# Kernel tuning notes

Hardware: AMD Instinct MI355X
Metric: run time of the kernel (lower is better)

Reference implementation:

```python
import jax, jax.numpy as jnp
import numpy as np
from jax import lax


def setup_inputs() -> dict:
    key = jax.random.key(0)
    k1, k2 = jax.random.split(key)
    C, H, W = 64, 224, 224
    C_out, hf, wf = 128, 3, 3
    x = jax.random.normal(k1, (C, H, W), dtype=jnp.float32)
    kernels = jax.random.normal(k2, (C_out, C, hf, wf), dtype=jnp.float32)
    return {"x": x, "kernels": kernels}


def reference(x, kernels):
    # Original builds im2col columns per output pixel then does k_col @ x_col,
    # i.e. a cross-correlation with 'valid' padding and stride 1.
    # lax.conv_general_dilated computes exactly this (no kernel flip).
    stride = 1
    out = lax.conv_general_dilated(
        x[None],                       # (1, C, H, W) NCHW
        kernels,                       # (C_out, C_in, hf, wf) OIHW
        window_strides=(stride, stride),
        padding="VALID",
        dimension_numbers=("NCHW", "OIHW", "NCHW"),
    )
    return out[0]                      # (C_out, H_out, W_out)
```

## Files before the change

kernel.cpp:

```cpp
#include <hip/hip_runtime.h>
#include <hip/hip_bf16.h>


#define H_IN   224
#define W_IN   224
#define C_OUT  128
#define H_OUT  222
#define W_OUT  222
#define XP     226
#define CPAD   72
#define TW     68

typedef __attribute__((ext_vector_type(8)))  short bf16x8;
typedef __attribute__((ext_vector_type(16))) float f32x16;

static __device__ __forceinline__ unsigned short f2bs(float f) {
    union { __hip_bfloat16 h; unsigned short u; } cv;
    cv.h = __float2bfloat16(f);
    return cv.u;
}

__global__ __launch_bounds__(256)
void transform_w_kernel(const float* __restrict__ w, __hip_bfloat16* __restrict__ wt)
{
    int idx = blockIdx.x * 256 + threadIdx.x;
    if (idx < 9 * 128 * 64) {
        int ij  = idx >> 13;
        int rem = idx & 8191;
        int co  = rem >> 6;
        int c   = rem & 63;
        wt[((ij * 8 + (c >> 3)) * 128 + co) * 8 + (c & 7)] =
            __float2bfloat16(w[(co * 64 + c) * 9 + ij]);
    }
}

__global__ __launch_bounds__(256)
void transpose_x_kernel(const float* __restrict__ x, __hip_bfloat16* __restrict__ xt)
{
    __shared__ __align__(16) unsigned short tile[64 * TW];
    const int h  = blockIdx.y;
    const int w0 = blockIdx.x * 64;
    const int t  = threadIdx.x;

    {
        const int wq = (t & 15) * 4;
        const int c0 = t >> 4;
        #pragma unroll
        for (int p = 0; p < 4; ++p) {
            const int c  = c0 + p * 16;
            const int wg = w0 + wq;
            float4 v = make_float4(0.f, 0.f, 0.f, 0.f);
            if (h < H_IN && wg < W_IN)
                v = *(const float4*)(x + ((size_t)c * H_IN + h) * W_IN + wg);
            ushort4 b;
            b.x = f2bs(v.x); b.y = f2bs(v.y); b.z = f2bs(v.z); b.w = f2bs(v.w);
            *(ushort4*)(tile + c * TW + wq) = b;
        }
    }
    __syncthreads();

    {
        const int wl = t >> 2;
        const int cq = (t & 3) * 16;
        const int wg = w0 + wl;
        if (wg < XP) {
            alignas(16) unsigned short r[16];
            #pragma unroll
            for (int k = 0; k < 16; ++k)
                r[k] = tile[(cq + k) * TW + wl];
            float4* d = (float4*)((unsigned short*)xt + ((size_t)h * XP + wg) * 64 + cq);
            d[0] = ((const float4*)r)[0];
            d[1] = ((const float4*)r)[1];
        }
    }
}

__global__ __launch_bounds__(256)
void conv_mfma_kernel(const __hip_bfloat16* __restrict__ xt,
                      const __hip_bfloat16* __restrict__ wt,
                      float* __restrict__ out)
{
    __shared__ __hip_bfloat16 xs[10 * 34 * CPAD];
    __shared__ __hip_bfloat16 wsb[2][8 * 64 * 8];
    const int ow0 = blockIdx.x * 32;
    const int oh0 = blockIdx.y * 8;
    const int co0 = blockIdx.z * 64;
    const int tid = threadIdx.x;

    for (int q = tid; q < 10 * 34 * 8; q += 256) {
        int sub = q & 7;
        int pix = q >> 3;
        int row = pix / 34;
        int wc  = pix - row * 34;
        *(float4*)(xs + (row * 34 + wc) * CPAD + sub * 8) =
            *(const float4*)(xt + ((oh0 + row) * XP + (ow0 + wc)) * 64 + sub * 8);
    }
    {
        const float4* s = (const float4*)(wt + (size_t)co0 * 8);
        #pragma unroll
        for (int k = 0; k < 2; ++k) {
            int q  = k * 256 + tid;
            int ks = q >> 6;
            int cc = q & 63;
            *(float4*)(&wsb[0][(ks * 64 + cc) * 8]) =
                *(const float4*)(wt + ((0 * 8 + ks) * 128 + co0 + cc) * 8);
        }
        (void)s;
    }
    __syncthreads();

    const int wave = tid >> 6;
    const int lane = tid & 63;
    const int n    = lane & 31;
    const int h    = lane >> 5;
    const int r0   = wave * 2;

    f32x16 acc[2][2] = {};

    #pragma unroll
    for (int p = 0; p < 9; ++p) {
        const int i  = p / 3;
        const int jj = p - i * 3;
        const int cb = p & 1;

        float4 pf[2];
        int ks0 = 0, cc0 = 0, ks1 = 0, cc1 = 0;
        if (p < 8) {
            #pragma unroll
            for (int k = 0; k < 2; ++k) {
                int q  = k * 256 + tid;
                int ks = q >> 6;
                int cc = q & 63;
                pf[k] = *(const float4*)(wt + (((p + 1) * 8 + ks) * 128 + co0 + cc) * 8);
                if (k == 0) { ks0 = ks; cc0 = cc; } else { ks1 = ks; cc1 = cc; }
            }
        }

        #pragma unroll
        for (int t = 0; t < 4; ++t) {
            bf16x8 afr[2], bfr[2];
            #pragma unroll
            for (int mi = 0; mi < 2; ++mi)
                afr[mi] = *(const bf16x8*)(&wsb[cb][((t * 2 + h) * 64 + mi * 32 + n) * 8]);
            #pragma unroll
            for (int ni = 0; ni < 2; ++ni)
                bfr[ni] = *(const bf16x8*)(xs +
                    ((i + r0 + ni) * 34 + n + jj) * CPAD + t * 16 + h * 8);
            #pragma unroll
            for (int mi = 0; mi < 2; ++mi)
                #pragma unroll
                for (int ni = 0; ni < 2; ++ni)
                    acc[mi][ni] = __builtin_amdgcn_mfma_f32_32x32x16_bf16(
                        afr[mi], bfr[ni], acc[mi][ni], 0, 0, 0);
        }

        if (p < 8) {
            *(float4*)(&wsb[1 - cb][(ks0 * 64 + cc0) * 8]) = pf[0];
            *(float4*)(&wsb[1 - cb][(ks1 * 64 + cc1) * 8]) = pf[1];
        }
        __syncthreads();
    }

    #pragma unroll
    for (int mi = 0; mi < 2; ++mi) {
        #pragma unroll
        for (int ni = 0; ni < 2; ++ni) {
            const int oh = oh0 + r0 + ni;
            const int ow = ow0 + n;
            if (oh < H_OUT && ow < W_OUT) {
                #pragma unroll
                for (int r = 0; r < 16; ++r) {
                    int co = co0 + mi * 32 + (r & 3) + 8 * (r >> 2) + 4 * h;
                    out[(size_t)co * (H_OUT * W_OUT) + oh * W_OUT + ow] = acc[mi][ni][r];
                }
            }
        }
    }
}

extern "C" void kernel_launch(void* const* d_in, const int* in_sizes, int n_in,
                              void* d_out, int out_size, void* d_ws, size_t ws_size,
                              hipStream_t stream)
{
    const float* x = (const float*)d_in[0];
    const float* w = (const float*)d_in[1];
    float* out     = (float*)d_out;

    __hip_bfloat16* xt = (__hip_bfloat16*)d_ws;
    __hip_bfloat16* wt = (__hip_bfloat16*)((char*)d_ws + (size_t)XP * XP * 64 * 2);

    transform_w_kernel<<<288, 256, 0, stream>>>(w, wt);
    transpose_x_kernel<<<dim3(4, XP), 256, 0, stream>>>(x, xt);
    conv_mfma_kernel<<<dim3(7, 28, 2), 256, 0, stream>>>(xt, wt, out);
}
```

Measured before the change: 88.64 us.

## Fuse weight/input preprocessing and conv into one cooperative kernel with grid sync

Merges the weight transform, input transpose and MFMA convolution kernels into a single cooperative launch of 512 blocks. The blocks first grid-stride over the preprocessing work units, reusing the shared-memory tile buffer, then a grid-wide sync separates that phase from the conv phase, which runs on the first 392 blocks. This removes two kernel launches and the gaps between them. In exchange it adds a grid barrier, requires co-residency (launch bounds of 2 blocks per CU), and leaves blocks idle during the conv phase.

Result: slower. 166.0 us (+87.3%).

```diff
diff --git a/kernel.cpp b/kernel.cpp
--- a/kernel.cpp
+++ b/kernel.cpp
@@ -1,5 +1,8 @@
 #include <hip/hip_runtime.h>
 #include <hip/hip_bf16.h>
+#include <hip/hip_cooperative_groups.h>
+
+namespace cg = cooperative_groups;
 
 
 #define H_IN   224
@@ -11,6 +14,11 @@
 #define CPAD   72
 #define TW     68
 
+#define PREP_W_UNITS 288
+#define PREP_UNITS   1192
+#define CONV_UNITS   392
+#define GRID_BLKS    512
+
 typedef __attribute__((ext_vector_type(8)))  short bf16x8;
 typedef __attribute__((ext_vector_type(16))) float f32x16;
 
@@ -20,72 +28,76 @@
     return cv.u;
 }
 
-__global__ __launch_bounds__(256)
-void transform_w_kernel(const float* __restrict__ w, __hip_bfloat16* __restrict__ wt)
+__global__ __launch_bounds__(256, 2)
+void fused_conv_kernel(const float* __restrict__ x, const float* __restrict__ w,
+                       __hip_bfloat16* __restrict__ xt, __hip_bfloat16* __restrict__ wt,
+                       float* __restrict__ out)
 {
-    int idx = blockIdx.x * 256 + threadIdx.x;
-    if (idx < 9 * 128 * 64) {
-        int ij  = idx >> 13;
-        int rem = idx & 8191;
-        int co  = rem >> 6;
-        int c   = rem & 63;
-        wt[((ij * 8 + (c >> 3)) * 128 + co) * 8 + (c & 7)] =
-            __float2bfloat16(w[(co * 64 + c) * 9 + ij]);
-    }
-}
-
-__global__ __launch_bounds__(256)
-void transpose_x_kernel(const float* __restrict__ x, __hip_bfloat16* __restrict__ xt)
-{
-    __shared__ __align__(16) unsigned short tile[64 * TW];
-    const int h  = blockIdx.y;
-    const int w0 = blockIdx.x * 64;
-    const int t  = threadIdx.x;
-
-    {
-        const int wq = (t & 15) * 4;
-        const int c0 = t >> 4;
-        #pragma unroll
-        for (int p = 0; p < 4; ++p) {
-            const int c  = c0 + p * 16;
-            const int wg = w0 + wq;
-            float4 v = make_float4(0.f, 0.f, 0.f, 0.f);
-            if (h < H_IN && wg < W_IN)
-                v = *(const float4*)(x + ((size_t)c * H_IN + h) * W_IN + wg);
-            ushort4 b;
-            b.x = f2bs(v.x); b.y = f2bs(v.y); b.z = f2bs(v.z); b.w = f2bs(v.w);
-            *(ushort4*)(tile + c * TW + wq) = b;
-        }
-    }
-    __syncthreads();
-
-    {
-        const int wl = t >> 2;
-        const int cq = (t & 3) * 16;
-        const int wg = w0 + wl;
-        if (wg < XP) {
-            alignas(16) unsigned short r[16];
-            #pragma unroll
-            for (int k = 0; k < 16; ++k)
-                r[k] = tile[(cq + k) * TW + wl];
-            float4* d = (float4*)((unsigned short*)xt + ((size_t)h * XP + wg) * 64 + cq);
-            d[0] = ((const float4*)r)[0];
-            d[1] = ((const float4*)r)[1];
-        }
-    }
-}
-
-__global__ __launch_bounds__(256)
-void conv_mfma_kernel(const __hip_bfloat16* __restrict__ xt,
-                      const __hip_bfloat16* __restrict__ wt,
-                      float* __restrict__ out)
-{
-    __shared__ __hip_bfloat16 xs[10 * 34 * CPAD];
-    __shared__ __hip_bfloat16 wsb[2][8 * 64 * 8];
-    const int ow0 = blockIdx.x * 32;
-    const int oh0 = blockIdx.y * 8;
-    const int co0 = blockIdx.z * 64;
+    __shared__ __align__(16) __hip_bfloat16 xs[10 * 34 * CPAD];
+    __shared__ __align__(16) __hip_bfloat16 wsb[2][8 * 64 * 8];
     const int tid = threadIdx.x;
+
+    for (int u = blockIdx.x; u < PREP_UNITS; u += GRID_BLKS) {
+        if (u < PREP_W_UNITS) {
+            int idx = u * 256 + tid;
+            int ij  = idx >> 13;
+            int rem = idx & 8191;
+            int co  = rem >> 6;
+            int c   = rem & 63;
+            wt[((ij * 8 + (c >> 3)) * 128 + co) * 8 + (c & 7)] =
+                __float2bfloat16(w[(co * 64 + c) * 9 + ij]);
+        } else {
+            unsigned short* tile = (unsigned short*)xs;
+            const int ux = u - PREP_W_UNITS;
+            const int h  = ux >> 2;
+            const int w0 = (ux & 3) * 64;
+            __syncthreads();
+
+            {
+                const int wq = (tid & 15) * 4;
+                const int c0 = tid >> 4;
+                #pragma unroll
+                for (int p = 0; p < 4; ++p) {
+                    const int c  = c0 + p * 16;
+                    const int wg = w0 + wq;
+                    float4 v = make_float4(0.f, 0.f, 0.f, 0.f);
+                    if (h < H_IN && wg < W_IN)
+                        v = *(const float4*)(x + ((size_t)c * H_IN + h) * W_IN + wg);
+                    ushort4 b;
+                    b.x = f2bs(v.x); b.y = f2bs(v.y); b.z = f2bs(v.z); b.w = f2bs(v.w);
+                    *(ushort4*)(tile + c * TW + wq) = b;
+                }
+            }
+            __syncthreads();
+
+            {
+                const int wl = tid >> 2;
+                const int cq = (tid & 3) * 16;
+                const int wg = w0 + wl;
+                if (wg < XP) {
+                    alignas(16) unsigned short r[16];
+                    #pragma unroll
+                    for (int k = 0; k < 16; ++k)
+                        r[k] = tile[(cq + k) * TW + wl];
+                    float4* d = (float4*)((unsigned short*)xt + ((size_t)h * XP + wg) * 64 + cq);
+                    d[0] = ((const float4*)r)[0];
+                    d[1] = ((const float4*)r)[1];
+                }
+            }
+        }
+    }
+
+    cg::this_grid().sync();
+
+    const int u = blockIdx.x;
+    if (u >= CONV_UNITS) return;
+    const int bz  = u / 196;
+    const int rm  = u - bz * 196;
+    const int by  = rm / 7;
+    const int bx  = rm - by * 7;
+    const int ow0 = bx * 32;
+    const int oh0 = by * 8;
+    const int co0 = bz * 64;
 
     for (int q = tid; q < 10 * 34 * 8; q += 256) {
         int sub = q & 7;
@@ -95,17 +107,13 @@
         *(float4*)(xs + (row * 34 + wc) * CPAD + sub * 8) =
             *(const float4*)(xt + ((oh0 + row) * XP + (ow0 + wc)) * 64 + sub * 8);
     }
-    {
-        const float4* s = (const float4*)(wt + (size_t)co0 * 8);
-        #pragma unroll
-        for (int k = 0; k < 2; ++k) {
-            int q  = k * 256 + tid;
-            int ks = q >> 6;
-            int cc = q & 63;
-            *(float4*)(&wsb[0][(ks * 64 + cc) * 8]) =
-                *(const float4*)(wt + ((0 * 8 + ks) * 128 + co0 + cc) * 8);
-        }
-        (void)s;
+    #pragma unroll
+    for (int k = 0; k < 2; ++k) {
+        int q  = k * 256 + tid;
+        int ks = q >> 6;
+        int cc = q & 63;
+        *(float4*)(&wsb[0][(ks * 64 + cc) * 8]) =
+            *(const float4*)(wt + ((0 * 8 + ks) * 128 + co0 + cc) * 8);
     }
     __syncthreads();
 
@@ -189,7 +197,7 @@
     __hip_bfloat16* xt = (__hip_bfloat16*)d_ws;
     __hip_bfloat16* wt = (__hip_bfloat16*)((char*)d_ws + (size_t)XP * XP * 64 * 2);
 
-    transform_w_kernel<<<288, 256, 0, stream>>>(w, wt);
-    transpose_x_kernel<<<dim3(4, XP), 256, 0, stream>>>(x, xt);
-    conv_mfma_kernel<<<dim3(7, 28, 2), 256, 0, stream>>>(xt, wt, out);
+    void* args[] = { (void*)&x, (void*)&w, (void*)&xt, (void*)&wt, (void*)&out };
+    hipLaunchCooperativeKernel(fused_conv_kernel, dim3(GRID_BLKS), dim3(256),
+                               args, 0, stream);
 }
```

## Halve output-row tile, load weights directly from global, drop LDS weight buffer

Applied to the files above, without the earlier changes.

The conv kernel now handles 4 output rows per block instead of 8, doubling the grid, and each wave computes one row instead of two. Weight fragments are read straight from global memory (cached) instead of being double-buffered through shared memory, which removes the per-tap __syncthreads barriers. A launch bounds occupancy hint is added. The aim is higher occupancy and less synchronisation, at the cost of more halo reloads, fewer MFMAs per weight load and global-latency weight fetches in the inner loop.

Measured after the change: 88.01 us. About the same (-0.7%).

```diff
diff --git a/kernel.cpp b/kernel.cpp
--- a/kernel.cpp
+++ b/kernel.cpp
@@ -75,19 +75,18 @@
     }
 }
 
-__global__ __launch_bounds__(256)
+__global__ __launch_bounds__(256, 4)
 void conv_mfma_kernel(const __hip_bfloat16* __restrict__ xt,
                       const __hip_bfloat16* __restrict__ wt,
                       float* __restrict__ out)
 {
-    __shared__ __hip_bfloat16 xs[10 * 34 * CPAD];
-    __shared__ __hip_bfloat16 wsb[2][8 * 64 * 8];
+    __shared__ __hip_bfloat16 xs[6 * 34 * CPAD];
     const int ow0 = blockIdx.x * 32;
-    const int oh0 = blockIdx.y * 8;
+    const int oh0 = blockIdx.y * 4;
     const int co0 = blockIdx.z * 64;
     const int tid = threadIdx.x;
 
-    for (int q = tid; q < 10 * 34 * 8; q += 256) {
+    for (int q = tid; q < 6 * 34 * 8; q += 256) {
         int sub = q & 7;
         int pix = q >> 3;
         int row = pix / 34;
@@ -95,84 +94,44 @@
         *(float4*)(xs + (row * 34 + wc) * CPAD + sub * 8) =
             *(const float4*)(xt + ((oh0 + row) * XP + (ow0 + wc)) * 64 + sub * 8);
     }
-    {
-        const float4* s = (const float4*)(wt + (size_t)co0 * 8);
-        #pragma unroll
-        for (int k = 0; k < 2; ++k) {
-            int q  = k * 256 + tid;
-            int ks = q >> 6;
-            int cc = q & 63;
-            *(float4*)(&wsb[0][(ks * 64 + cc) * 8]) =
-                *(const float4*)(wt + ((0 * 8 + ks) * 128 + co0 + cc) * 8);
-        }
-        (void)s;
-    }
     __syncthreads();
 
     const int wave = tid >> 6;
     const int lane = tid & 63;
     const int n    = lane & 31;
     const int h    = lane >> 5;
-    const int r0   = wave * 2;
 
-    f32x16 acc[2][2] = {};
+    f32x16 acc[2] = {};
 
     #pragma unroll
     for (int p = 0; p < 9; ++p) {
         const int i  = p / 3;
         const int jj = p - i * 3;
-        const int cb = p & 1;
-
-        float4 pf[2];
-        int ks0 = 0, cc0 = 0, ks1 = 0, cc1 = 0;
-        if (p < 8) {
-            #pragma unroll
-            for (int k = 0; k < 2; ++k) {
-                int q  = k * 256 + tid;
-                int ks = q >> 6;
-                int cc = q & 63;
-                pf[k] = *(const float4*)(wt + (((p + 1) * 8 + ks) * 128 + co0 + cc) * 8);
-                if (k == 0) { ks0 = ks; cc0 = cc; } else { ks1 = ks; cc1 = cc; }
-            }
-        }
-
         #pragma unroll
         for (int t = 0; t < 4; ++t) {
-            bf16x8 afr[2], bfr[2];
+            bf16x8 afr[2];
             #pragma unroll
             for (int mi = 0; mi < 2; ++mi)
-                afr[mi] = *(const bf16x8*)(&wsb[cb][((t * 2 + h) * 64 + mi * 32 + n) * 8]);
-            #pragma unroll
-            for (int ni = 0; ni < 2; ++ni)
-                bfr[ni] = *(const bf16x8*)(xs +
-                    ((i + r0 + ni) * 34 + n + jj) * CPAD + t * 16 + h * 8);
+                afr[mi] = *(const bf16x8*)(wt +
+                    (size_t)(((p * 8 + t * 2 + h) * 128 + co0 + mi * 32 + n) * 8));
+            bf16x8 bfr = *(const bf16x8*)(xs +
+                ((i + wave) * 34 + n + jj) * CPAD + t * 16 + h * 8);
             #pragma unroll
             for (int mi = 0; mi < 2; ++mi)
-                #pragma unroll
-                for (int ni = 0; ni < 2; ++ni)
-                    acc[mi][ni] = __builtin_amdgcn_mfma_f32_32x32x16_bf16(
-                        afr[mi], bfr[ni], acc[mi][ni], 0, 0, 0);
+                acc[mi] = __builtin_amdgcn_mfma_f32_32x32x16_bf16(
+                    afr[mi], bfr, acc[mi], 0, 0, 0);
         }
-
-        if (p < 8) {
-            *(float4*)(&wsb[1 - cb][(ks0 * 64 + cc0) * 8]) = pf[0];
-            *(float4*)(&wsb[1 - cb][(ks1 * 64 + cc1) * 8]) = pf[1];
-        }
-        __syncthreads();
     }
 
-    #pragma unroll
-    for (int mi = 0; mi < 2; ++mi) {
+    const int oh = oh0 + wave;
+    const int ow = ow0 + n;
+    if (oh < H_OUT && ow < W_OUT) {
         #pragma unroll
-        for (int ni = 0; ni < 2; ++ni) {
-            const int oh = oh0 + r0 + ni;
-            const int ow = ow0 + n;
-            if (oh < H_OUT && ow < W_OUT) {
-                #pragma unroll
-                for (int r = 0; r < 16; ++r) {
-                    int co = co0 + mi * 32 + (r & 3) + 8 * (r >> 2) + 4 * h;
-                    out[(size_t)co * (H_OUT * W_OUT) + oh * W_OUT + ow] = acc[mi][ni][r];
-                }
+        for (int mi = 0; mi < 2; ++mi) {
+            #pragma unroll
+            for (int r = 0; r < 16; ++r) {
+                int co = co0 + mi * 32 + (r & 3) + 8 * (r >> 2) + 4 * h;
+                out[(size_t)co * (H_OUT * W_OUT) + oh * W_OUT + ow] = acc[mi][r];
             }
         }
     }
@@ -191,5 +150,5 @@
 
     transform_w_kernel<<<288, 256, 0, stream>>>(w, wt);
     transpose_x_kernel<<<dim3(4, XP), 256, 0, stream>>>(x, xt);
-    conv_mfma_kernel<<<dim3(7, 28, 2), 256, 0, stream>>>(xt, wt, out);
+    conv_mfma_kernel<<<dim3(7, 56, 2), 256, 0, stream>>>(xt, wt, out);
 }
```
